# Performance work log

Hardware: AMD Instinct MI355X
Metric: run time of the kernel (lower is better)

Reference implementation:

```python
import jax, jax.numpy as jnp
import numpy as np
import math

HIDDEN = 1024
NUM_HEADS = 16
HEAD_DIM = HIDDEN // NUM_HEADS
B, S = 4, 1024


def setup_inputs() -> dict:
    key = jax.random.key(0)
    ks = jax.random.split(key, 16)
    sd = 1.0 / math.sqrt(HIDDEN)
    inp = {
        "x": jax.random.normal(ks[0], (B, S, HIDDEN), jnp.float32),
        "spikes": jax.random.uniform(ks[1], (B, S, HIDDEN), jnp.float32),
        "membrane_potential": jax.random.normal(ks[2], (B, S, HIDDEN), jnp.float32),
        "Wq": jax.random.normal(ks[3], (HIDDEN, HIDDEN), jnp.float32) * sd,
        "bq": jnp.zeros((HIDDEN,), jnp.float32),
        "Wk": jax.random.normal(ks[4], (HIDDEN, HIDDEN), jnp.float32) * sd,
        "bk": jnp.zeros((HIDDEN,), jnp.float32),
        "Wv": jax.random.normal(ks[5], (HIDDEN, HIDDEN), jnp.float32) * sd,
        "bv": jnp.zeros((HIDDEN,), jnp.float32),
        "Wo": jax.random.normal(ks[6], (HIDDEN, HIDDEN), jnp.float32) * sd,
        "bo": jnp.zeros((HIDDEN,), jnp.float32),
        "tau_decay": jnp.ones((NUM_HEADS,), jnp.float32) * 10.0,
        "Wg": jax.random.normal(ks[7], (HIDDEN, 2 * HIDDEN), jnp.float32) * sd,
        "bg": jnp.zeros((HIDDEN,), jnp.float32),
    }
    return inp


def _heads(t):  # [B,S,H] -> [B,nH,S,hd]
    Bv, Sv, _ = t.shape
    return t.reshape(Bv, Sv, NUM_HEADS, HEAD_DIM).transpose(0, 2, 1, 3)


def reference(x, spikes, membrane_potential, Wq, bq, Wk, bk, Wv, bv, Wo, bo, tau_decay, Wg, bg):
    scale = 1.0 / math.sqrt(HEAD_DIM)
    q = _heads(x @ Wq.T + bq)
    k = _heads(x @ Wk.T + bk)
    v = _heads(x @ Wv.T + bv)

    # raw scores [B,nH,S,S]
    scores = jnp.einsum('bhqd,bhkd->bhqk', q, k) * scale

    # per-head exponential temporal decay mask [nH,S,S]
    times = jnp.arange(S, dtype=jnp.float32)
    tdiff = jnp.abs(times[:, None] - times[None, :])  # [S,S]
    tmask = jnp.exp(-tdiff[None] / tau_decay[:, None, None])
    scores = scores * tmask[None]

    # spike correlation term
    sm = _heads(spikes)
    spike_attn = jnp.einsum('bhqd,bhkd->bhqk', sm, sm) * scale
    scores = scores * (1.0 + spike_attn)

    # membrane gating of V
    v = v * jax.nn.sigmoid(_heads(membrane_potential))

    probs = jax.nn.softmax(scores, axis=-1)
    context = jnp.einsum('bhqk,bhkd->bhqd', probs, v)
    context = context.transpose(0, 2, 1, 3).reshape(B, S, HIDDEN)

    # dendritic gate
    gate_in = jnp.concatenate([context, membrane_potential], axis=-1)
    gate = jax.nn.sigmoid(gate_in @ Wg.T + bg)
    context = context * gate

    return context @ Wo.T + bo
```

## Files before the change

### kernel.cpp

```cpp
#include <hip/hip_runtime.h>
#include <math.h>
#include <stdint.h>

namespace {

typedef __attribute__((ext_vector_type(8))) short s8v;
typedef __attribute__((ext_vector_type(4))) float f4v;
typedef unsigned short u16;

__device__ __forceinline__ float fexp2(float x) {
  return __builtin_amdgcn_exp2f(x);
}

__device__ __forceinline__ u16 f2bf(float f) {
  union { float f; uint32_t u; } v; v.f = f;
  uint32_t r = v.u + 0x7fffu + ((v.u >> 16) & 1u);
  return (u16)(r >> 16);
}
__device__ __forceinline__ float bf2f(u16 h) {
  union { uint32_t u; float f; } v; v.u = ((uint32_t)h) << 16;
  return v.f;
}
__device__ __forceinline__ uint32_t pk2r(float a, float b) {
  return (uint32_t)f2bf(a) | ((uint32_t)f2bf(b) << 16);
}
__device__ __forceinline__ uint32_t pk2(float a, float b) {
  union { float f; uint32_t u; } x, y; x.f = a; y.f = b;
  return ((x.u + 0x8000u) >> 16) | ((y.u + 0x8000u) & 0xffff0000u);
}
__device__ __forceinline__ float sigmoidf_(float x) { return 1.0f / (1.0f + __expf(-x)); }

__device__ __forceinline__ void gload16(const u16* g, u16* l) {
  __builtin_amdgcn_global_load_lds(
      (const __attribute__((address_space(1))) void*)g,
      (__attribute__((address_space(3))) void*)l, 16, 0, 0);
}

struct CvtJob { const float* src; u16* dst; };
struct CvtArgs { CvtJob j[18]; float* vz; };

__global__ __launch_bounds__(256) void cvt_kernel(CvtArgs a) {
  if (blockIdx.y == 0 && blockIdx.x < 4) {
    float4 z; z.x = 0.f; z.y = 0.f; z.z = 0.f; z.w = 0.f;
    ((float4*)a.vz)[blockIdx.x * 256 + threadIdx.x] = z;
  }
  const CvtJob jb = a.j[blockIdx.y];
  const int i = blockIdx.x * 256 + threadIdx.x;
  const float4 v = ((const float4*)jb.src)[i];
  uint2 pk;
  pk.x = pk2r(v.x, v.y);
  pk.y = pk2r(v.z, v.w);
  ((uint2*)jb.dst)[i] = pk;
}

__global__ __launch_bounds__(512, 2) void qkv_gemm(
    const u16* __restrict__ xb,
    const u16* __restrict__ Wqb, const u16* __restrict__ Wkb, const u16* __restrict__ Wvb,
    const float* __restrict__ bq, const float* __restrict__ bk, const float* __restrict__ bv,
    const float* __restrict__ mem,
    u16* __restrict__ Qb, u16* __restrict__ Kb, u16* __restrict__ Vt,
    float* __restrict__ Vtot) {
  __shared__ __align__(16) u16 as_[4][4096];
  __shared__ __align__(16) u16 bs_[4][12288];
  const int t = threadIdx.x;
  const int nb = blockIdx.x, mb = blockIdx.y;
  const int m0 = mb * 128, n0 = nb * 128;
  const int l = t & 63, w = t >> 6;
  const int wm = w >> 2, wn = w & 3;
  const int lr = l & 15, lq = l >> 4;
  const int rh = lr >> 1;
  const int rb4 = (lr & 1) << 2;

  const f4v fz = {0.f, 0.f, 0.f, 0.f};
  f4v aq[4][2], ak[4][2], av[4][2];
#pragma unroll
  for (int i = 0; i < 4; ++i)
#pragma unroll
    for (int j = 0; j < 2; ++j) { aq[i][j] = fz; ak[i][j] = fz; av[i][j] = fz; }

  const int tt = t & 255, uu = t >> 8;
  const int sc0 = (tt & 7) ^ ((tt >> 3) & 7);
  const int sgrow = ((tt >> 3) << 1) + (sc0 >> 2);
  const int sgk = (sc0 & 3) << 3;

  const u16* ga = xb + (size_t)(m0 + uu * 64 + sgrow) * 1024 + sgk;
  const u16* gq = Wqb + (size_t)(n0 + uu * 64 + sgrow) * 1024 + sgk;
  const u16* gk = Wkb + (size_t)(n0 + uu * 64 + sgrow) * 1024 + sgk;
  const u16* gv = Wvb + (size_t)(n0 + uu * 64 + sgrow) * 1024 + sgk;
  const int lofs = uu * 2048 + tt * 8;

#define STAGE_A(c) gload16(ga + (c) * 32, &as_[(c) & 3][lofs])
#define STAGE_Q(c) gload16(gq + (c) * 32, &bs_[(c) & 3][lofs])
#define STAGE_K(c) gload16(gk + (c) * 32, &bs_[(c) & 3][4096 + lofs])
#define STAGE_V(c) gload16(gv + (c) * 32, &bs_[(c) & 3][8192 + lofs])

  STAGE_A(0); STAGE_Q(0); STAGE_K(0); STAGE_V(0);
  STAGE_A(1); STAGE_Q(1); STAGE_K(1); STAGE_V(1);
  STAGE_A(2); STAGE_Q(2); STAGE_K(2); STAGE_V(2);
  asm volatile("s_waitcnt vmcnt(8)" ::: "memory");
  __builtin_amdgcn_s_barrier();

  const int co = ((rb4 + lq) ^ rh) * 8;
  for (int c = 0; c < 32; ++c) {
    const int cb = c & 3;
    const bool st = (c + 3 < 32);
    s8v af[4], bq2[2];
#pragma unroll
    for (int mi = 0; mi < 4; ++mi)
      af[mi] = *(const s8v*)(&as_[cb][(wm * 32 + mi * 8 + rh) * 64 + co]);
#pragma unroll
    for (int ni = 0; ni < 2; ++ni)
      bq2[ni] = *(const s8v*)(&bs_[cb][(wn * 16 + ni * 8 + rh) * 64 + co]);
    if (st) { STAGE_A(c + 3); STAGE_Q(c + 3); }
    __builtin_amdgcn_s_barrier();
    asm volatile("s_waitcnt lgkmcnt(0)" ::: "memory");
    __builtin_amdgcn_sched_barrier(0);
    __builtin_amdgcn_s_setprio(1);
#pragma unroll
    for (int mi = 0; mi < 4; ++mi)
#pragma unroll
      for (int ni = 0; ni < 2; ++ni)
        aq[mi][ni] = __builtin_amdgcn_mfma_f32_16x16x32_bf16(
            bq2[ni], af[mi], aq[mi][ni], 0, 0, 0);
    __builtin_amdgcn_s_setprio(0);
    s8v bk2[2];
#pragma unroll
    for (int ni = 0; ni < 2; ++ni)
      bk2[ni] = *(const s8v*)(&bs_[cb][4096 + (wn * 16 + ni * 8 + rh) * 64 + co]);
    if (st) STAGE_K(c + 3);
    __builtin_amdgcn_s_barrier();
    asm volatile("s_waitcnt lgkmcnt(0)" ::: "memory");
    __builtin_amdgcn_sched_barrier(0);
    __builtin_amdgcn_s_setprio(1);
#pragma unroll
    for (int mi = 0; mi < 4; ++mi)
#pragma unroll
      for (int ni = 0; ni < 2; ++ni)
        ak[mi][ni] = __builtin_amdgcn_mfma_f32_16x16x32_bf16(
            bk2[ni], af[mi], ak[mi][ni], 0, 0, 0);
    __builtin_amdgcn_s_setprio(0);
    s8v bv2[2];
#pragma unroll
    for (int ni = 0; ni < 2; ++ni)
      bv2[ni] = *(const s8v*)(&bs_[cb][8192 + (wn * 16 + ni * 8 + rh) * 64 + co]);
    if (st) STAGE_V(c + 3);
    __builtin_amdgcn_s_barrier();
    asm volatile("s_waitcnt lgkmcnt(0)" ::: "memory");
    __builtin_amdgcn_sched_barrier(0);
    __builtin_amdgcn_s_setprio(1);
#pragma unroll
    for (int mi = 0; mi < 4; ++mi)
#pragma unroll
      for (int ni = 0; ni < 2; ++ni)
        av[mi][ni] = __builtin_amdgcn_mfma_f32_16x16x32_bf16(
            af[mi], bv2[ni], av[mi][ni], 0, 0, 0);
    __builtin_amdgcn_s_setprio(0);
    if (st) {
      asm volatile("s_waitcnt vmcnt(8)" ::: "memory");
    } else if (c == 29) {
      asm volatile("s_waitcnt vmcnt(4)" ::: "memory");
    } else if (c == 30) {
      asm volatile("s_waitcnt vmcnt(0)" ::: "memory");
    }
    if (c < 31) __builtin_amdgcn_s_barrier();
  }
#undef STAGE_A
#undef STAGE_Q
#undef STAGE_K
#undef STAGE_V
  __builtin_amdgcn_sched_barrier(0);

#pragma unroll
  for (int mi = 0; mi < 4; ++mi)
#pragma unroll
    for (int ni = 0; ni < 2; ++ni) {
      const int m = m0 + wm * 64 + mi * 16 + lr;
      const int nb4 = n0 + wn * 32 + ni * 16 + lq * 4;
      const float4 b4 = *(const float4*)&bq[nb4];
      uint2 pk;
      pk.x = pk2r(aq[mi][ni][0] + b4.x, aq[mi][ni][1] + b4.y);
      pk.y = pk2r(aq[mi][ni][2] + b4.z, aq[mi][ni][3] + b4.w);
      *(uint2*)(Qb + (size_t)m * 1024 + nb4) = pk;
    }
#pragma unroll
  for (int mi = 0; mi < 4; ++mi)
#pragma unroll
    for (int ni = 0; ni < 2; ++ni) {
      const int m = m0 + wm * 64 + mi * 16 + lr;
      const int nb4 = n0 + wn * 32 + ni * 16 + lq * 4;
      const float4 b4 = *(const float4*)&bk[nb4];
      uint2 pk;
      pk.x = pk2r(ak[mi][ni][0] + b4.x, ak[mi][ni][1] + b4.y);
      pk.y = pk2r(ak[mi][ni][2] + b4.z, ak[mi][ni][3] + b4.w);
      *(uint2*)(Kb + (size_t)m * 1024 + nb4) = pk;
    }
  {
    const int b = m0 >> 10;
    float vpart[2] = {0.f, 0.f};
#pragma unroll
    for (int mi = 0; mi < 4; ++mi)
#pragma unroll
      for (int ni = 0; ni < 2; ++ni) {
        const int mrow = m0 + wm * 64 + mi * 16 + lq * 4;
        const int ncol = n0 + wn * 32 + ni * 16 + lr;
        const int h = ncol >> 6, d = ncol & 63;
        const float bi = bv[ncol];
        float tv[4];
#pragma unroll
        for (int r = 0; r < 4; ++r)
          tv[r] = (av[mi][ni][r] + bi) * sigmoidf_(mem[(size_t)(mrow + r) * 1024 + ncol]);
        vpart[ni] += (tv[0] + tv[1]) + (tv[2] + tv[3]);
        const int s = mrow & 1023;
        uint2 pk;
        pk.x = pk2r(tv[0], tv[1]);
        pk.y = pk2r(tv[2], tv[3]);
        *(uint2*)(Vt + ((size_t)((b * 16 + h) * 64 + d)) * 1024 + s) = pk;
      }
#pragma unroll
    for (int ni = 0; ni < 2; ++ni) {
      const int ncol = n0 + wn * 32 + ni * 16 + lr;
      atomicAdd(&Vtot[(size_t)(b * 16 + (ncol >> 6)) * 64 + (ncol & 63)], vpart[ni]);
    }
  }
}

template <int MODE>
__global__ __launch_bounds__(512, 2) void gemm64(
    const u16* __restrict__ Ab, const u16* __restrict__ A2b,
    const u16* __restrict__ W, const float* __restrict__ bias,
    u16* __restrict__ outb, float* __restrict__ outf, int K) {
  __shared__ __align__(16) u16 as_[4][4096], bs_[4][4096];
  const int t = threadIdx.x;
  const int m0 = blockIdx.y * 128, n0 = blockIdx.x * 128;
  const int l = t & 63, w = t >> 6;
  const int wm = w >> 2, wn = w & 3;
  const int lr = l & 15, lq = l >> 4;
  const int rh = lr >> 1, rb4 = (lr & 1) << 2;
  const f4v fz = {0.f, 0.f, 0.f, 0.f};
  f4v acc[4][2];
#pragma unroll
  for (int i = 0; i < 4; ++i)
#pragma unroll
    for (int j = 0; j < 2; ++j) acc[i][j] = fz;

  const int tt = t & 255, uu = t >> 8;
  const int sc0 = (tt & 7) ^ ((tt >> 3) & 7);
  const int sgrow = ((tt >> 3) << 1) + (sc0 >> 2);
  const int sgk = (sc0 & 3) << 3;
  const u16* ga1 = Ab + (size_t)(m0 + uu * 64 + sgrow) * 1024 + sgk;
  const u16* ga2 = (MODE == 1)
      ? (A2b + (size_t)(m0 + uu * 64 + sgrow) * 1024 + sgk) : ga1;
  const u16* gw = W + (size_t)(n0 + uu * 64 + sgrow) * K + sgk;
  const int lofs = uu * 2048 + tt * 8;
  const int nc = K >> 5;

#define G_STAGE_A(c)                                                           \
  {                                                                            \
    const int ko_ = (c) * 32;                                                  \
    if (MODE == 1 && ko_ >= 1024) gload16(ga2 + (ko_ - 1024), &as_[(c) & 3][lofs]); \
    else gload16(ga1 + ko_, &as_[(c) & 3][lofs]);                              \
  }
#define G_STAGE_W(c) gload16(gw + (c) * 32, &bs_[(c) & 3][lofs])

  G_STAGE_A(0); G_STAGE_W(0);
  G_STAGE_A(1); G_STAGE_W(1);
  G_STAGE_A(2); G_STAGE_W(2);
  asm volatile("s_waitcnt vmcnt(4)" ::: "memory");
  __builtin_amdgcn_s_barrier();

  const int co = ((rb4 + lq) ^ rh) * 8;
  for (int c = 0; c < nc; ++c) {
    const int cb = c & 3;
    s8v af[4], bf[2];
#pragma unroll
    for (int mi = 0; mi < 4; ++mi)
      af[mi] = *(const s8v*)(&as_[cb][(wm * 32 + mi * 8 + rh) * 64 + co]);
#pragma unroll
    for (int ni = 0; ni < 2; ++ni)
      bf[ni] = *(const s8v*)(&bs_[cb][(wn * 16 + ni * 8 + rh) * 64 + co]);
    if (c + 3 < nc) { G_STAGE_A(c + 3); G_STAGE_W(c + 3); }
    __builtin_amdgcn_s_barrier();
    asm volatile("s_waitcnt lgkmcnt(0)" ::: "memory");
    __builtin_amdgcn_sched_barrier(0);
    __builtin_amdgcn_s_setprio(1);
#pragma unroll
    for (int mi = 0; mi < 4; ++mi)
#pragma unroll
      for (int ni = 0; ni < 2; ++ni)
        acc[mi][ni] = __builtin_amdgcn_mfma_f32_16x16x32_bf16(
            bf[ni], af[mi], acc[mi][ni], 0, 0, 0);
    __builtin_amdgcn_s_setprio(0);
    if (c + 3 < nc) {
      asm volatile("s_waitcnt vmcnt(4)" ::: "memory");
    } else if (c + 3 == nc) {
      asm volatile("s_waitcnt vmcnt(2)" ::: "memory");
    } else if (c + 2 == nc) {
      asm volatile("s_waitcnt vmcnt(0)" ::: "memory");
    }
    if (c + 1 < nc) __builtin_amdgcn_s_barrier();
  }
#undef G_STAGE_A
#undef G_STAGE_W
  __builtin_amdgcn_sched_barrier(0);

#pragma unroll
  for (int mi = 0; mi < 4; ++mi)
#pragma unroll
    for (int ni = 0; ni < 2; ++ni) {
      const int m = m0 + wm * 64 + mi * 16 + lr;
      const int nb4 = n0 + wn * 32 + ni * 16 + lq * 4;
      const float4 b4 = *(const float4*)&bias[nb4];
      if (MODE == 0) {
        float4 o;
        o.x = acc[mi][ni][0] + b4.x; o.y = acc[mi][ni][1] + b4.y;
        o.z = acc[mi][ni][2] + b4.z; o.w = acc[mi][ni][3] + b4.w;
        *(float4*)(outf + (size_t)m * 1024 + nb4) = o;
      } else {
        const uint2 a2 = *(const uint2*)(Ab + (size_t)m * 1024 + nb4);
        float cx[4] = {bf2f((u16)(a2.x & 0xffff)), bf2f((u16)(a2.x >> 16)),
                       bf2f((u16)(a2.y & 0xffff)), bf2f((u16)(a2.y >> 16))};
        float g[4];
        g[0] = cx[0] * sigmoidf_(acc[mi][ni][0] + b4.x);
        g[1] = cx[1] * sigmoidf_(acc[mi][ni][1] + b4.y);
        g[2] = cx[2] * sigmoidf_(acc[mi][ni][2] + b4.z);
        g[3] = cx[3] * sigmoidf_(acc[mi][ni][3] + b4.w);
        uint2 pk;
        pk.x = pk2r(g[0], g[1]);
        pk.y = pk2r(g[2], g[3]);
        *(uint2*)(outb + (size_t)m * 1024 + nb4) = pk;
      }
    }
}

__global__ __launch_bounds__(256) void attn_mfma(
    const u16* __restrict__ Qb, const u16* __restrict__ Kb,
    const u16* __restrict__ SPb, const u16* __restrict__ Vt,
    const float* __restrict__ tau, const float* __restrict__ Vtot,
    u16* __restrict__ CTXb) {
  __shared__ u16 kbuf[4096], skbuf[4096], vbuf[4096];
  __shared__ u16 pbuf[4][16 * 64];
  const int t = threadIdx.x, l = t & 63, w = t >> 6;
  const int lr = l & 15, lq = l >> 4;
  const int p = blockIdx.x;
  const int g = (p & 7) + 8 * (p >> 7);
  const int qt = (p >> 3) & 15;
  const int h = g & 15, b = g >> 4;

  const float tv_ = tau[h];
  const float c2 = 1.44269504088896f / tv_;
  const float K0 = 0.125f * 1.44269504088896f;
  int rad = (int)ceilf(tv_ * 0.171875f);
  if (rad > 15) rad = 15;
  const int jlo = (qt - rad < 0) ? 0 : qt - rad;
  const int jhi = (qt + rad > 15) ? 15 : qt + rad;
  const int farCnt = 16 - (jhi - jlo + 1);

  float cN[4], cNi[4], cR[4], cRi[4];
#pragma unroll
  for (int i = 0; i < 4; ++i) {
    cN[i]  = fexp2(c2 * (float)(i * 16));
    cNi[i] = fexp2(-c2 * (float)(i * 16));
    cR[i]  = fexp2(c2 * (float)(lq * 4 + i));
    cRi[i] = fexp2(-c2 * (float)(lq * 4 + i));
  }

  s8v qf[2], sf[2];
  {
    const size_t base = ((size_t)(b * 1024 + qt * 64 + w * 16 + lr)) * 1024 + h * 64 + lq * 8;
    qf[0] = *(const s8v*)(Qb + base);
    qf[1] = *(const s8v*)(Qb + base + 32);
    sf[0] = *(const s8v*)(SPb + base);
    sf[1] = *(const s8v*)(SPb + base + 32);
  }
  const s8v ones = {0x3F80, 0x3F80, 0x3F80, 0x3F80, 0x3F80, 0x3F80, 0x3F80, 0x3F80};

  const f4v fz = {0.f, 0.f, 0.f, 0.f};
  f4v oacc[4], vs[4];
  float lacc[4];
#pragma unroll
  for (int i = 0; i < 4; ++i) { oacc[i] = fz; vs[i] = fz; lacc[i] = 0.f; }

  const int iqw = qt * 64 + w * 16;
  const int srow = t >> 3;
  const int csw = ((t & 7) ^ (srow & 7)) * 8;
  const int rx = lr & 7;
  u16* pw = pbuf[w];

  for (int jc = jlo; jc <= jhi; ++jc) {
    const int j0 = jc * 64;
    __syncthreads();
    {
      const size_t kg = ((size_t)(b * 1024 + j0 + srow)) * 1024 + h * 64 + csw;
      gload16(Kb + kg, kbuf + t * 8);
      gload16(Kb + kg + 32 * 1024, kbuf + 2048 + t * 8);
      gload16(SPb + kg, skbuf + t * 8);
      gload16(SPb + kg + 32 * 1024, skbuf + 2048 + t * 8);
      const size_t vg = ((size_t)((b * 16 + h) * 64 + srow)) * 1024 + j0 + csw;
      gload16(Vt + vg, vbuf + t * 8);
      gload16(Vt + vg + 32 * 1024, vbuf + 2048 + t * 8);
    }
    __syncthreads();

    f4v sa[4], ssa[4];
#pragma unroll
    for (int ni = 0; ni < 4; ++ni) { sa[ni] = fz; ssa[ni] = fz; }
#pragma unroll
    for (int ks = 0; ks < 2; ++ks) {
#pragma unroll
      for (int ni = 0; ni < 4; ++ni) {
        const int off = (ni * 16 + lr) * 64 + (((ks * 4 + lq) ^ rx) * 8);
        const s8v kf = *(const s8v*)(kbuf + off);
        sa[ni] = __builtin_amdgcn_mfma_f32_16x16x32_bf16(kf, qf[ks], sa[ni], 0, 0, 0);
        const s8v skf = *(const s8v*)(skbuf + off);
        ssa[ni] = __builtin_amdgcn_mfma_f32_16x16x32_bf16(skf, sf[ks], ssa[ni], 0, 0, 0);
      }
    }

    const int D0 = iqw - j0;
    float pv[4][4];
    if (jc < qt) {
      const float EA = K0 * fexp2(-c2 * (float)(D0 + lr));
#pragma unroll
      for (int ni = 0; ni < 4; ++ni)
#pragma unroll
        for (int r = 0; r < 4; ++r) {
          const float t1 = fmaf(ssa[ni][r], 0.125f, 1.0f);
          const float e = fexp2(sa[ni][r] * cN[ni] * cR[r] * EA * t1);
          pv[ni][r] = e;
          lacc[ni] += e;
        }
    } else if (jc > qt) {
      const float EAi = K0 * fexp2(c2 * (float)(D0 + lr));
#pragma unroll
      for (int ni = 0; ni < 4; ++ni)
#pragma unroll
        for (int r = 0; r < 4; ++r) {
          const float t1 = fmaf(ssa[ni][r], 0.125f, 1.0f);
          const float e = fexp2(sa[ni][r] * cNi[ni] * cRi[r] * EAi * t1);
          pv[ni][r] = e;
          lacc[ni] += e;
        }
    } else {
      const float EA  = K0 * fexp2(-c2 * (float)(D0 + lr));
      const float EAi = K0 * fexp2(c2 * (float)(D0 + lr));
#pragma unroll
      for (int ni = 0; ni < 4; ++ni)
#pragma unroll
        for (int r = 0; r < 4; ++r) {
          const int jloc = ni * 16 + lq * 4 + r;
          const float fb = cN[ni] * cR[r] * EA;
          const float fa = cNi[ni] * cRi[r] * EAi;
          const float f = (D0 + lr >= jloc) ? fb : fa;
          const float t1 = fmaf(ssa[ni][r], 0.125f, 1.0f);
          const float e = fexp2(sa[ni][r] * f * t1);
          pv[ni][r] = e;
          lacc[ni] += e;
        }
    }

#pragma unroll
    for (int ni = 0; ni < 4; ++ni) {
      const int phys = (ni * 2 + (lq >> 1)) ^ rx;
      uint2 p2;
      p2.x = pk2(pv[ni][0], pv[ni][1]);
      p2.y = pk2(pv[ni][2], pv[ni][3]);
      *(uint2*)(pw + lr * 64 + phys * 8 + (lq & 1) * 4) = p2;
    }

#pragma unroll
    for (int ks = 0; ks < 2; ++ks) {
      const s8v pf = *(const s8v*)(pw + lr * 64 + (((ks * 4 + lq) ^ rx) * 8));
#pragma unroll
      for (int nd = 0; nd < 4; ++nd) {
        const int off = (nd * 16 + lr) * 64 + (((ks * 4 + lq) ^ rx) * 8);
        const s8v vf = *(const s8v*)(vbuf + off);
        oacc[nd] = __builtin_amdgcn_mfma_f32_16x16x32_bf16(vf, pf, oacc[nd], 0, 0, 0);
        vs[nd] = __builtin_amdgcn_mfma_f32_16x16x32_bf16(vf, ones, vs[nd], 0, 0, 0);
      }
    }
  }

  float ls = (lacc[0] + lacc[1]) + (lacc[2] + lacc[3]);
  ls += __shfl_xor(ls, 16);
  ls += __shfl_xor(ls, 32);
  ls += 64.0f * (float)farCnt;
  const float inv = 1.0f / ls;
  const float* vt0 = Vtot + (size_t)(b * 16 + h) * 64;
  const size_t orow = ((size_t)(b * 1024 + qt * 64 + w * 16 + lr)) * 1024 + h * 64;
#pragma unroll
  for (int nd = 0; nd < 4; ++nd) {
    const float4 vt4 = *(const float4*)(vt0 + nd * 16 + lq * 4);
    float o0 = (oacc[nd][0] + vt4.x - vs[nd][0]) * inv;
    float o1 = (oacc[nd][1] + vt4.y - vs[nd][1]) * inv;
    float o2 = (oacc[nd][2] + vt4.z - vs[nd][2]) * inv;
    float o3 = (oacc[nd][3] + vt4.w - vs[nd][3]) * inv;
    uint2 o;
    o.x = pk2r(o0, o1);
    o.y = pk2r(o2, o3);
    *(uint2*)(CTXb + orow + nd * 16 + lq * 4) = o;
  }
}

}

extern "C" void kernel_launch(void* const* d_in, const int* in_sizes, int n_in,
                              void* d_out, int out_size, void* d_ws, size_t ws_size,
                              hipStream_t stream) {
  const float* x      = (const float*)d_in[0];
  const float* spikes = (const float*)d_in[1];
  const float* mem    = (const float*)d_in[2];
  const float* Wq     = (const float*)d_in[3];
  const float* bq     = (const float*)d_in[4];
  const float* Wk     = (const float*)d_in[5];
  const float* bk     = (const float*)d_in[6];
  const float* Wv     = (const float*)d_in[7];
  const float* bv     = (const float*)d_in[8];
  const float* Wo     = (const float*)d_in[9];
  const float* bo     = (const float*)d_in[10];
  const float* tau    = (const float*)d_in[11];
  const float* Wg     = (const float*)d_in[12];
  const float* bg     = (const float*)d_in[13];
  float* out = (float*)d_out;

  uint8_t* w8 = (uint8_t*)d_ws;
  u16* spb  = (u16*)(w8);
  u16* xb   = (u16*)(w8 + (8u << 20));
  u16* Wqb  = (u16*)(w8 + (16u << 20));
  u16* Wkb  = (u16*)(w8 + (18u << 20));
  u16* Wvb  = (u16*)(w8 + (20u << 20));
  u16* Wob  = (u16*)(w8 + (22u << 20));
  u16* Wgb  = (u16*)(w8 + (24u << 20));
  u16* Qb   = (u16*)(w8 + (28u << 20));
  u16* Kb   = (u16*)(w8 + (36u << 20));
  u16* Vt   = (u16*)(w8 + (44u << 20));
  u16* CTXb = (u16*)(w8 + (52u << 20));
  float* Vtot = (float*)(w8 + (60u << 20));
  u16* memb = (u16*)d_out;
  u16* gctx = xb;

  constexpr size_t QE = 262144 * 4;
  CvtArgs ca;
  for (int q = 0; q < 4; ++q) ca.j[q]     = {x + q * QE,      xb + q * QE};
  for (int q = 0; q < 4; ++q) ca.j[4 + q] = {spikes + q * QE, spb + q * QE};
  for (int q = 0; q < 4; ++q) ca.j[8 + q] = {mem + q * QE,    memb + q * QE};
  ca.j[12] = {Wq, Wqb};
  ca.j[13] = {Wk, Wkb};
  ca.j[14] = {Wv, Wvb};
  ca.j[15] = {Wo, Wob};
  ca.j[16] = {Wg, Wgb};
  ca.j[17] = {Wg + QE, Wgb + QE};
  ca.vz = Vtot;
  cvt_kernel<<<dim3(1024, 18), 256, 0, stream>>>(ca);

  qkv_gemm<<<dim3(8, 32), 512, 0, stream>>>(xb, Wqb, Wkb, Wvb, bq, bk, bv, mem,
                                            Qb, Kb, Vt, Vtot);
  attn_mfma<<<dim3(1024), 256, 0, stream>>>(Qb, Kb, spb, Vt, tau, Vtot, CTXb);
  gemm64<1><<<dim3(8, 32), 512, 0, stream>>>(CTXb, memb, Wgb, bg, gctx, nullptr, 2048);
  gemm64<0><<<dim3(8, 32), 512, 0, stream>>>(gctx, nullptr, Wob, bo, nullptr, out, 1024);
}
```

Before: 253.9 us.

## Split QKV GEMM into per-matrix warp groups with 768-thread blocks

The fused QKV projection kernel now uses 12 waves per block, with each group of 4 waves owning one of Q, K or V, in place of 8 waves that cycled through all three matrices in sequence. Each K-step needs one barrier instead of three, and each wave holds a larger 64x64 accumulator tile. The V epilogue also reads the bf16 copy of the membrane potential instead of the fp32 one, which halves that read traffic. In exchange, only 512 of the 768 threads issue global loads, register pressure per wave rises under the 768-thread launch bound, and the sigmoid gate now sees bf16-rounded inputs.

```diff
diff --git a/kernel.cpp b/kernel.cpp
--- a/kernel.cpp
+++ b/kernel.cpp
@@ -53,11 +53,11 @@
   ((uint2*)jb.dst)[i] = pk;
 }
 
-__global__ __launch_bounds__(512, 2) void qkv_gemm(
+__global__ __launch_bounds__(768, 3) void qkv_gemm(
     const u16* __restrict__ xb,
     const u16* __restrict__ Wqb, const u16* __restrict__ Wkb, const u16* __restrict__ Wvb,
     const float* __restrict__ bq, const float* __restrict__ bk, const float* __restrict__ bv,
-    const float* __restrict__ mem,
+    const u16* __restrict__ memb,
     u16* __restrict__ Qb, u16* __restrict__ Kb, u16* __restrict__ Vt,
     float* __restrict__ Vtot) {
   __shared__ __align__(16) u16 as_[4][4096];
@@ -66,22 +66,25 @@
   const int nb = blockIdx.x, mb = blockIdx.y;
   const int m0 = mb * 128, n0 = nb * 128;
   const int l = t & 63, w = t >> 6;
-  const int wm = w >> 2, wn = w & 3;
+  const int mat = w >> 2;
+  const int wl = w & 3, wm = wl >> 1, wn = wl & 1;
   const int lr = l & 15, lq = l >> 4;
   const int rh = lr >> 1;
   const int rb4 = (lr & 1) << 2;
+  const int bmat = mat * 4096;
 
   const f4v fz = {0.f, 0.f, 0.f, 0.f};
-  f4v aq[4][2], ak[4][2], av[4][2];
+  f4v acc[4][4];
 #pragma unroll
   for (int i = 0; i < 4; ++i)
 #pragma unroll
-    for (int j = 0; j < 2; ++j) { aq[i][j] = fz; ak[i][j] = fz; av[i][j] = fz; }
-
-  const int tt = t & 255, uu = t >> 8;
+    for (int j = 0; j < 4; ++j) acc[i][j] = fz;
+
+  const int tt = t & 255, uu = (t >> 8) & 1;
   const int sc0 = (tt & 7) ^ ((tt >> 3) & 7);
   const int sgrow = ((tt >> 3) << 1) + (sc0 >> 2);
   const int sgk = (sc0 & 3) << 3;
+  const bool stg = (t < 512);
 
   const u16* ga = xb + (size_t)(m0 + uu * 64 + sgrow) * 1024 + sgk;
   const u16* gq = Wqb + (size_t)(n0 + uu * 64 + sgrow) * 1024 + sgk;
@@ -89,14 +92,17 @@
   const u16* gv = Wvb + (size_t)(n0 + uu * 64 + sgrow) * 1024 + sgk;
   const int lofs = uu * 2048 + tt * 8;
 
-#define STAGE_A(c) gload16(ga + (c) * 32, &as_[(c) & 3][lofs])
-#define STAGE_Q(c) gload16(gq + (c) * 32, &bs_[(c) & 3][lofs])
-#define STAGE_K(c) gload16(gk + (c) * 32, &bs_[(c) & 3][4096 + lofs])
-#define STAGE_V(c) gload16(gv + (c) * 32, &bs_[(c) & 3][8192 + lofs])
-
-  STAGE_A(0); STAGE_Q(0); STAGE_K(0); STAGE_V(0);
-  STAGE_A(1); STAGE_Q(1); STAGE_K(1); STAGE_V(1);
-  STAGE_A(2); STAGE_Q(2); STAGE_K(2); STAGE_V(2);
+#define QKV_STAGE(c)                                                           \
+  {                                                                            \
+    const int ko_ = (c) * 32;                                                  \
+    const int bb_ = (c) & 3;                                                   \
+    gload16(ga + ko_, &as_[bb_][lofs]);                                        \
+    gload16(gq + ko_, &bs_[bb_][lofs]);                                        \
+    gload16(gk + ko_, &bs_[bb_][4096 + lofs]);                                 \
+    gload16(gv + ko_, &bs_[bb_][8192 + lofs]);                                 \
+  }
+
+  if (stg) { QKV_STAGE(0); QKV_STAGE(1); QKV_STAGE(2); }
   asm volatile("s_waitcnt vmcnt(8)" ::: "memory");
   __builtin_amdgcn_s_barrier();
 
@@ -104,56 +110,33 @@
   for (int c = 0; c < 32; ++c) {
     const int cb = c & 3;
     const bool st = (c + 3 < 32);
-    s8v af[4], bq2[2];
+    s8v af[4], bf[4];
 #pragma unroll
     for (int mi = 0; mi < 4; ++mi)
       af[mi] = *(const s8v*)(&as_[cb][(wm * 32 + mi * 8 + rh) * 64 + co]);
 #pragma unroll
-    for (int ni = 0; ni < 2; ++ni)
-      bq2[ni] = *(const s8v*)(&bs_[cb][(wn * 16 + ni * 8 + rh) * 64 + co]);
-    if (st) { STAGE_A(c + 3); STAGE_Q(c + 3); }
+    for (int ni = 0; ni < 4; ++ni)
+      bf[ni] = *(const s8v*)(&bs_[cb][bmat + (wn * 32 + ni * 8 + rh) * 64 + co]);
+    if (stg && st) QKV_STAGE(c + 3);
     __builtin_amdgcn_s_barrier();
     asm volatile("s_waitcnt lgkmcnt(0)" ::: "memory");
     __builtin_amdgcn_sched_barrier(0);
     __builtin_amdgcn_s_setprio(1);
-#pragma unroll
-    for (int mi = 0; mi < 4; ++mi)
-#pragma unroll
-      for (int ni = 0; ni < 2; ++ni)
-        aq[mi][ni] = __builtin_amdgcn_mfma_f32_16x16x32_bf16(
-            bq2[ni], af[mi], aq[mi][ni], 0, 0, 0);
-    __builtin_amdgcn_s_setprio(0);
-    s8v bk2[2];
-#pragma unroll
-    for (int ni = 0; ni < 2; ++ni)
-      bk2[ni] = *(const s8v*)(&bs_[cb][4096 + (wn * 16 + ni * 8 + rh) * 64 + co]);
-    if (st) STAGE_K(c + 3);
-    __builtin_amdgcn_s_barrier();
-    asm volatile("s_waitcnt lgkmcnt(0)" ::: "memory");
-    __builtin_amdgcn_sched_barrier(0);
-    __builtin_amdgcn_s_setprio(1);
-#pragma unroll
-    for (int mi = 0; mi < 4; ++mi)
-#pragma unroll
-      for (int ni = 0; ni < 2; ++ni)
-        ak[mi][ni] = __builtin_amdgcn_mfma_f32_16x16x32_bf16(
-            bk2[ni], af[mi], ak[mi][ni], 0, 0, 0);
-    __builtin_amdgcn_s_setprio(0);
-    s8v bv2[2];
-#pragma unroll
-    for (int ni = 0; ni < 2; ++ni)
-      bv2[ni] = *(const s8v*)(&bs_[cb][8192 + (wn * 16 + ni * 8 + rh) * 64 + co]);
-    if (st) STAGE_V(c + 3);
-    __builtin_amdgcn_s_barrier();
-    asm volatile("s_waitcnt lgkmcnt(0)" ::: "memory");
-    __builtin_amdgcn_sched_barrier(0);
-    __builtin_amdgcn_s_setprio(1);
-#pragma unroll
-    for (int mi = 0; mi < 4; ++mi)
-#pragma unroll
-      for (int ni = 0; ni < 2; ++ni)
-        av[mi][ni] = __builtin_amdgcn_mfma_f32_16x16x32_bf16(
-            af[mi], bv2[ni], av[mi][ni], 0, 0, 0);
+    if (mat < 2) {
+#pragma unroll
+      for (int mi = 0; mi < 4; ++mi)
+#pragma unroll
+        for (int ni = 0; ni < 4; ++ni)
+          acc[mi][ni] = __builtin_amdgcn_mfma_f32_16x16x32_bf16(
+              bf[ni], af[mi], acc[mi][ni], 0, 0, 0);
+    } else {
+#pragma unroll
+      for (int mi = 0; mi < 4; ++mi)
+#pragma unroll
+        for (int ni = 0; ni < 4; ++ni)
+          acc[mi][ni] = __builtin_amdgcn_mfma_f32_16x16x32_bf16(
+              af[mi], bf[ni], acc[mi][ni], 0, 0, 0);
+    }
     __builtin_amdgcn_s_setprio(0);
     if (st) {
       asm volatile("s_waitcnt vmcnt(8)" ::: "memory");
@@ -164,51 +147,40 @@
     }
     if (c < 31) __builtin_amdgcn_s_barrier();
   }
-#undef STAGE_A
-#undef STAGE_Q
-#undef STAGE_K
-#undef STAGE_V
+#undef QKV_STAGE
   __builtin_amdgcn_sched_barrier(0);
 
-#pragma unroll
-  for (int mi = 0; mi < 4; ++mi)
-#pragma unroll
-    for (int ni = 0; ni < 2; ++ni) {
-      const int m = m0 + wm * 64 + mi * 16 + lr;
-      const int nb4 = n0 + wn * 32 + ni * 16 + lq * 4;
-      const float4 b4 = *(const float4*)&bq[nb4];
-      uint2 pk;
-      pk.x = pk2r(aq[mi][ni][0] + b4.x, aq[mi][ni][1] + b4.y);
-      pk.y = pk2r(aq[mi][ni][2] + b4.z, aq[mi][ni][3] + b4.w);
-      *(uint2*)(Qb + (size_t)m * 1024 + nb4) = pk;
-    }
-#pragma unroll
-  for (int mi = 0; mi < 4; ++mi)
-#pragma unroll
-    for (int ni = 0; ni < 2; ++ni) {
-      const int m = m0 + wm * 64 + mi * 16 + lr;
-      const int nb4 = n0 + wn * 32 + ni * 16 + lq * 4;
-      const float4 b4 = *(const float4*)&bk[nb4];
-      uint2 pk;
-      pk.x = pk2r(ak[mi][ni][0] + b4.x, ak[mi][ni][1] + b4.y);
-      pk.y = pk2r(ak[mi][ni][2] + b4.z, ak[mi][ni][3] + b4.w);
-      *(uint2*)(Kb + (size_t)m * 1024 + nb4) = pk;
-    }
-  {
+  if (mat < 2) {
+    u16* dst = (mat == 0) ? Qb : Kb;
+    const float* bias = (mat == 0) ? bq : bk;
+#pragma unroll
+    for (int mi = 0; mi < 4; ++mi)
+#pragma unroll
+      for (int ni = 0; ni < 4; ++ni) {
+        const int m = m0 + wm * 64 + mi * 16 + lr;
+        const int nb4 = n0 + wn * 64 + ni * 16 + lq * 4;
+        const float4 b4 = *(const float4*)&bias[nb4];
+        uint2 pk;
+        pk.x = pk2r(acc[mi][ni][0] + b4.x, acc[mi][ni][1] + b4.y);
+        pk.y = pk2r(acc[mi][ni][2] + b4.z, acc[mi][ni][3] + b4.w);
+        *(uint2*)(dst + (size_t)m * 1024 + nb4) = pk;
+      }
+  } else {
     const int b = m0 >> 10;
-    float vpart[2] = {0.f, 0.f};
+    float vpart[4] = {0.f, 0.f, 0.f, 0.f};
 #pragma unroll
     for (int mi = 0; mi < 4; ++mi)
 #pragma unroll
-      for (int ni = 0; ni < 2; ++ni) {
+      for (int ni = 0; ni < 4; ++ni) {
         const int mrow = m0 + wm * 64 + mi * 16 + lq * 4;
-        const int ncol = n0 + wn * 32 + ni * 16 + lr;
+        const int ncol = n0 + wn * 64 + ni * 16 + lr;
         const int h = ncol >> 6, d = ncol & 63;
         const float bi = bv[ncol];
         float tv[4];
 #pragma unroll
         for (int r = 0; r < 4; ++r)
-          tv[r] = (av[mi][ni][r] + bi) * sigmoidf_(mem[(size_t)(mrow + r) * 1024 + ncol]);
+          tv[r] = (acc[mi][ni][r] + bi) *
+                  sigmoidf_(bf2f(memb[(size_t)(mrow + r) * 1024 + ncol]));
         vpart[ni] += (tv[0] + tv[1]) + (tv[2] + tv[3]);
         const int s = mrow & 1023;
         uint2 pk;
@@ -217,8 +189,8 @@
         *(uint2*)(Vt + ((size_t)((b * 16 + h) * 64 + d)) * 1024 + s) = pk;
       }
 #pragma unroll
-    for (int ni = 0; ni < 2; ++ni) {
-      const int ncol = n0 + wn * 32 + ni * 16 + lr;
+    for (int ni = 0; ni < 4; ++ni) {
+      const int ncol = n0 + wn * 64 + ni * 16 + lr;
       atomicAdd(&Vtot[(size_t)(b * 16 + (ncol >> 6)) * 64 + (ncol & 63)], vpart[ni]);
     }
   }
@@ -552,7 +524,7 @@
   ca.vz = Vtot;
   cvt_kernel<<<dim3(1024, 18), 256, 0, stream>>>(ca);
 
-  qkv_gemm<<<dim3(8, 32), 512, 0, stream>>>(xb, Wqb, Wkb, Wvb, bq, bk, bv, mem,
+  qkv_gemm<<<dim3(8, 32), 768, 0, stream>>>(xb, Wqb, Wkb, Wvb, bq, bk, bv, memb,
                                             Qb, Kb, Vt, Vtot);
   attn_mfma<<<dim3(1024), 256, 0, stream>>>(Qb, Kb, spb, Vt, tau, Vtot, CTXb);
   gemm64<1><<<dim3(8, 32), 512, 0, stream>>>(CTXb, memb, Wgb, bg, gctx, nullptr, 2048);
```

Result: no change. 254.2 us (+0.1%).
